# Performance work log

Hardware: AMD Instinct MI355X
Metric: run time of the kernel (lower is better)

## Reference

```python
import jax, jax.numpy as jnp
import numpy as np

B, K, T = 4096, 512, 30
TEMP = 1.0                 # args.score_temp
MAX_GUESSES = 6            # _MAX_GUESSES_NUM
MISS_THRESH = 2.0          # _MISSING_THRESHOLD


def setup_inputs() -> dict:
    key = jax.random.key(0)
    k1, k2, k3, k4 = jax.random.split(key, 4)
    return {
        "output": jax.random.normal(k1, (B * K, 1), dtype=jnp.float32),
        "pred_candidates": jax.random.normal(k2, (B, K, T, 2), dtype=jnp.float32),
        "pred_gt": jax.random.normal(k3, (B, T, 2), dtype=jnp.float32),
        "scales": jax.random.uniform(k4, (B,), dtype=jnp.float32, minval=0.5, maxval=2.0),
    }


def reference(output, pred_candidates, pred_gt, scales):
    out = output.reshape(B, K)                                   # per-sample candidate scores
    # scaled displacement norms: [B, K, T]
    diff = pred_candidates - pred_gt[:, None, :, :]
    disp = scales[:, None, None] * jnp.linalg.norm(diff, axis=-1)
    fde = disp[..., -1]                                          # [B, K] final displacement
    # ScoreEvaluator (FDE metric): higher score = closer endpoint
    scores = -fde
    # classification loss: CE between softmax(target/temp) and log_softmax(output), sum-reduced
    tgt = jax.nn.softmax(scores / TEMP, axis=1)
    logp = jax.nn.log_softmax(out, axis=1)
    cls_loss = -(tgt * logp).sum(axis=1)                         # [B]
    # miss loss: minFDE among top-6 scored candidates, hinged at threshold
    _, top_idx = jax.lax.top_k(out, MAX_GUESSES)                 # [B, 6]
    top_fde = jnp.take_along_axis(fde, top_idx, axis=1)          # [B, 6]
    miss_loss = jnp.maximum(top_fde.min(axis=1) - MISS_THRESH, 0.0)
    return (cls_loss + miss_loss).mean()
```

## Files before the change

kernel.cpp:

```cpp
#include <hip/hip_runtime.h>
#include <cmath>

constexpr int B  = 4096;
constexpr int K  = 512;
constexpr int T  = 30;
constexpr int NT = 256;
constexpr int PT = K / NT;
constexpr int NW = NT / 64;
constexpr int MAX_GUESSES  = 6;
constexpr float MISS_THRESH = 2.0f;

__global__ __launch_bounds__(NT) void score_classify_kernel(
    const float* __restrict__ outp,
    const float* __restrict__ cand,
    const float* __restrict__ gt,
    const float* __restrict__ scales,
    float* __restrict__ part)
{
    const int b    = blockIdx.x;
    const int tid  = threadIdx.x;
    const int wave = tid >> 6;
    const int lane = tid & 63;

    __shared__ float s_fde[K];
    __shared__ float s_red[3 * NW];
    __shared__ int   s_redi[NW];
    __shared__ float s_bcast[2];
    __shared__ int   s_bi;

    const float2 g  = *(const float2*)(gt + ((size_t)b * T + (T - 1)) * 2);
    const float  sc = scales[b];

    float o[PT], f[PT];
#pragma unroll
    for (int j = 0; j < PT; ++j) {
        const int k = tid + j * NT;
        const float2 c = *(const float2*)(cand + (((size_t)(b * K + k)) * T + (T - 1)) * 2);
        const float dx = c.x - g.x;
        const float dy = c.y - g.y;
        f[j] = sc * sqrtf(dx * dx + dy * dy);
        s_fde[k] = f[j];
        o[j] = outp[(size_t)b * K + k];
    }

    float m_o = fmaxf(o[0], o[1]);
    float m_s = fmaxf(-f[0], -f[1]);
    for (int off = 32; off >= 1; off >>= 1) {
        m_o = fmaxf(m_o, __shfl_down(m_o, off));
        m_s = fmaxf(m_s, __shfl_down(m_s, off));
    }
    if (lane == 0) { s_red[wave] = m_o; s_red[NW + wave] = m_s; }
    __syncthreads();
    if (tid == 0) {
        float a = s_red[0], c2 = s_red[NW];
        for (int w = 1; w < NW; ++w) {
            a  = fmaxf(a,  s_red[w]);
            c2 = fmaxf(c2, s_red[NW + w]);
        }
        s_bcast[0] = a; s_bcast[1] = c2;
    }
    __syncthreads();
    m_o = s_bcast[0];
    m_s = s_bcast[1];

    float zo = 0.f, zs = 0.f, ss = 0.f;
#pragma unroll
    for (int j = 0; j < PT; ++j) {
        zo += expf(o[j] - m_o);
        const float e = expf(-f[j] - m_s);
        zs += e;
        ss += e * o[j];
    }
    for (int off = 32; off >= 1; off >>= 1) {
        zo += __shfl_down(zo, off);
        zs += __shfl_down(zs, off);
        ss += __shfl_down(ss, off);
    }
    __syncthreads();
    if (lane == 0) { s_red[wave] = zo; s_red[NW + wave] = zs; s_red[2 * NW + wave] = ss; }
    __syncthreads();
    float cls = 0.f;
    if (tid == 0) {
        float tzo = 0.f, tzs = 0.f, tss = 0.f;
        for (int w = 0; w < NW; ++w) {
            tzo += s_red[w];
            tzs += s_red[NW + w];
            tss += s_red[2 * NW + w];
        }
        cls = m_o + logf(tzo) - tss / tzs;
    }

    bool used[PT];
#pragma unroll
    for (int j = 0; j < PT; ++j) used[j] = false;
    float minfde = 1e30f;

    for (int gidx = 0; gidx < MAX_GUESSES; ++gidx) {
        float bv = -1e30f;
        int   bi = 0x7fffffff;
#pragma unroll
        for (int j = 0; j < PT; ++j) {
            const int k = tid + j * NT;
            if (!used[j] && (o[j] > bv || (o[j] == bv && k < bi))) { bv = o[j]; bi = k; }
        }
        for (int off = 32; off >= 1; off >>= 1) {
            const float v2 = __shfl_down(bv, off);
            const int   i2 = __shfl_down(bi, off);
            if (v2 > bv || (v2 == bv && i2 < bi)) { bv = v2; bi = i2; }
        }
        __syncthreads();
        if (lane == 0) { s_red[wave] = bv; s_redi[wave] = bi; }
        __syncthreads();
        if (tid == 0) {
            float v = s_red[0]; int i = s_redi[0];
            for (int w = 1; w < NW; ++w) {
                if (s_red[w] > v || (s_red[w] == v && s_redi[w] < i)) { v = s_red[w]; i = s_redi[w]; }
            }
            s_bi = i;
        }
        __syncthreads();
        const int widx = s_bi;
        if ((widx & (NT - 1)) == tid) used[widx >> 8] = true;
        minfde = fminf(minfde, s_fde[widx]);
    }

    if (tid == 0) {
        const float miss = fmaxf(minfde - MISS_THRESH, 0.0f);
        part[b] = cls + miss;
    }
}

__global__ __launch_bounds__(NT) void reduce_mean_kernel(
    const float* __restrict__ part,
    float* __restrict__ result)
{
    const int tid  = threadIdx.x;
    const int wave = tid >> 6;
    const int lane = tid & 63;
    __shared__ float s_red[NW];

    float acc = 0.f;
#pragma unroll
    for (int i = tid; i < B; i += NT) acc += part[i];
    for (int off = 32; off >= 1; off >>= 1) acc += __shfl_down(acc, off);
    if (lane == 0) s_red[wave] = acc;
    __syncthreads();
    if (tid == 0) {
        float t = 0.f;
        for (int w = 0; w < NW; ++w) t += s_red[w];
        result[0] = t * (1.0f / (float)B);
    }
}

extern "C" void kernel_launch(void* const* d_in, const int* in_sizes, int n_in,
                              void* d_out, int out_size, void* d_ws, size_t ws_size,
                              hipStream_t stream) {
    const float* outp   = (const float*)d_in[0];
    const float* cand   = (const float*)d_in[1];
    const float* gt     = (const float*)d_in[2];
    const float* scales = (const float*)d_in[3];
    float* result = (float*)d_out;
    float* part   = (float*)d_ws;

    score_classify_kernel<<<B, NT, 0, stream>>>(outp, cand, gt, scales, part);
    reduce_mean_kernel<<<1, NT, 0, stream>>>(part, result);
}
```

Before: 617.2 us.

## Use one wavefront per sample with shuffle-only reductions and register top-k

The score kernel moves from a 256-thread block to a single 64-lane wavefront per sample, with 8 candidates per lane. All reductions (max, sums, the six top-k argmax rounds) become xor-shuffle butterflies, which removes the shared-memory staging and every __syncthreads. The winning candidate's FDE is fetched from registers with a lane shuffle instead of from a shared array. In exchange each lane does more serial work, and there are only 64 threads per block to hide the latency of the scattered 8-byte endpoint loads.

```diff
diff --git a/kernel.cpp b/kernel.cpp
--- a/kernel.cpp
+++ b/kernel.cpp
@@ -4,9 +4,8 @@
 constexpr int B  = 4096;
 constexpr int K  = 512;
 constexpr int T  = 30;
-constexpr int NT = 256;
+constexpr int NT = 64;
 constexpr int PT = K / NT;
-constexpr int NW = NT / 64;
 constexpr int MAX_GUESSES  = 6;
 constexpr float MISS_THRESH = 2.0f;
 
@@ -18,50 +17,39 @@
     float* __restrict__ part)
 {
     const int b    = blockIdx.x;
-    const int tid  = threadIdx.x;
-    const int wave = tid >> 6;
-    const int lane = tid & 63;
-
-    __shared__ float s_fde[K];
-    __shared__ float s_red[3 * NW];
-    __shared__ int   s_redi[NW];
-    __shared__ float s_bcast[2];
-    __shared__ int   s_bi;
+    const int lane = threadIdx.x;
 
     const float2 g  = *(const float2*)(gt + ((size_t)b * T + (T - 1)) * 2);
     const float  sc = scales[b];
 
-    float o[PT], f[PT];
+    float2 c[PT];
+    float  o[PT];
 #pragma unroll
     for (int j = 0; j < PT; ++j) {
-        const int k = tid + j * NT;
-        const float2 c = *(const float2*)(cand + (((size_t)(b * K + k)) * T + (T - 1)) * 2);
-        const float dx = c.x - g.x;
-        const float dy = c.y - g.y;
-        f[j] = sc * sqrtf(dx * dx + dy * dy);
-        s_fde[k] = f[j];
+        const int k = lane + j * NT;
+        c[j] = *(const float2*)(cand + (((size_t)(b * K + k)) * T + (T - 1)) * 2);
         o[j] = outp[(size_t)b * K + k];
     }
 
-    float m_o = fmaxf(o[0], o[1]);
-    float m_s = fmaxf(-f[0], -f[1]);
+    float f[PT];
+#pragma unroll
+    for (int j = 0; j < PT; ++j) {
+        const float dx = c[j].x - g.x;
+        const float dy = c[j].y - g.y;
+        f[j] = sc * sqrtf(dx * dx + dy * dy);
+    }
+
+    float m_o = o[0], m_s = -f[0];
+#pragma unroll
+    for (int j = 1; j < PT; ++j) {
+        m_o = fmaxf(m_o, o[j]);
+        m_s = fmaxf(m_s, -f[j]);
+    }
+#pragma unroll
     for (int off = 32; off >= 1; off >>= 1) {
-        m_o = fmaxf(m_o, __shfl_down(m_o, off));
-        m_s = fmaxf(m_s, __shfl_down(m_s, off));
+        m_o = fmaxf(m_o, __shfl_xor(m_o, off));
+        m_s = fmaxf(m_s, __shfl_xor(m_s, off));
     }
-    if (lane == 0) { s_red[wave] = m_o; s_red[NW + wave] = m_s; }
-    __syncthreads();
-    if (tid == 0) {
-        float a = s_red[0], c2 = s_red[NW];
-        for (int w = 1; w < NW; ++w) {
-            a  = fmaxf(a,  s_red[w]);
-            c2 = fmaxf(c2, s_red[NW + w]);
-        }
-        s_bcast[0] = a; s_bcast[1] = c2;
-    }
-    __syncthreads();
-    m_o = s_bcast[0];
-    m_s = s_bcast[1];
 
     float zo = 0.f, zs = 0.f, ss = 0.f;
 #pragma unroll
@@ -71,28 +59,15 @@
         zs += e;
         ss += e * o[j];
     }
+#pragma unroll
     for (int off = 32; off >= 1; off >>= 1) {
-        zo += __shfl_down(zo, off);
-        zs += __shfl_down(zs, off);
-        ss += __shfl_down(ss, off);
+        zo += __shfl_xor(zo, off);
+        zs += __shfl_xor(zs, off);
+        ss += __shfl_xor(ss, off);
     }
-    __syncthreads();
-    if (lane == 0) { s_red[wave] = zo; s_red[NW + wave] = zs; s_red[2 * NW + wave] = ss; }
-    __syncthreads();
-    float cls = 0.f;
-    if (tid == 0) {
-        float tzo = 0.f, tzs = 0.f, tss = 0.f;
-        for (int w = 0; w < NW; ++w) {
-            tzo += s_red[w];
-            tzs += s_red[NW + w];
-            tss += s_red[2 * NW + w];
-        }
-        cls = m_o + logf(tzo) - tss / tzs;
-    }
+    const float cls = m_o + logf(zo) - ss / zs;
 
-    bool used[PT];
-#pragma unroll
-    for (int j = 0; j < PT; ++j) used[j] = false;
+    unsigned used = 0;
     float minfde = 1e30f;
 
     for (int gidx = 0; gidx < MAX_GUESSES; ++gidx) {
@@ -100,54 +75,51 @@
         int   bi = 0x7fffffff;
 #pragma unroll
         for (int j = 0; j < PT; ++j) {
-            const int k = tid + j * NT;
-            if (!used[j] && (o[j] > bv || (o[j] == bv && k < bi))) { bv = o[j]; bi = k; }
+            const int k = lane + j * NT;
+            const bool ok = !(used & (1u << j));
+            if (ok && (o[j] > bv || (o[j] == bv && k < bi))) { bv = o[j]; bi = k; }
         }
+#pragma unroll
         for (int off = 32; off >= 1; off >>= 1) {
-            const float v2 = __shfl_down(bv, off);
-            const int   i2 = __shfl_down(bi, off);
+            const float v2 = __shfl_xor(bv, off);
+            const int   i2 = __shfl_xor(bi, off);
             if (v2 > bv || (v2 == bv && i2 < bi)) { bv = v2; bi = i2; }
         }
-        __syncthreads();
-        if (lane == 0) { s_red[wave] = bv; s_redi[wave] = bi; }
-        __syncthreads();
-        if (tid == 0) {
-            float v = s_red[0]; int i = s_redi[0];
-            for (int w = 1; w < NW; ++w) {
-                if (s_red[w] > v || (s_red[w] == v && s_redi[w] < i)) { v = s_red[w]; i = s_redi[w]; }
-            }
-            s_bi = i;
-        }
-        __syncthreads();
-        const int widx = s_bi;
-        if ((widx & (NT - 1)) == tid) used[widx >> 8] = true;
-        minfde = fminf(minfde, s_fde[widx]);
+        const int owner = bi & (NT - 1);
+        const int jw    = bi >> 6;
+        if (lane == owner) used |= (1u << jw);
+        float fv = f[0];
+#pragma unroll
+        for (int j = 1; j < PT; ++j) if (j == jw) fv = f[j];
+        const float wfde = __shfl(fv, owner);
+        minfde = fminf(minfde, wfde);
     }
 
-    if (tid == 0) {
+    if (lane == 0) {
         const float miss = fmaxf(minfde - MISS_THRESH, 0.0f);
         part[b] = cls + miss;
     }
 }
 
-__global__ __launch_bounds__(NT) void reduce_mean_kernel(
+__global__ __launch_bounds__(256) void reduce_mean_kernel(
     const float* __restrict__ part,
     float* __restrict__ result)
 {
     const int tid  = threadIdx.x;
     const int wave = tid >> 6;
     const int lane = tid & 63;
-    __shared__ float s_red[NW];
+    __shared__ float s_red[4];
 
     float acc = 0.f;
 #pragma unroll
-    for (int i = tid; i < B; i += NT) acc += part[i];
+    for (int i = tid; i < B; i += 256) acc += part[i];
+#pragma unroll
     for (int off = 32; off >= 1; off >>= 1) acc += __shfl_down(acc, off);
     if (lane == 0) s_red[wave] = acc;
     __syncthreads();
     if (tid == 0) {
         float t = 0.f;
-        for (int w = 0; w < NW; ++w) t += s_red[w];
+        for (int w = 0; w < 4; ++w) t += s_red[w];
         result[0] = t * (1.0f / (float)B);
     }
 }
@@ -163,5 +135,5 @@
     float* part   = (float*)d_ws;
 
     score_classify_kernel<<<B, NT, 0, stream>>>(outp, cand, gt, scales, part);
-    reduce_mean_kernel<<<1, NT, 0, stream>>>(part, result);
+    reduce_mean_kernel<<<1, 256, 0, stream>>>(part, result);
 }
```

Result: no change. 612.1 us (-0.8%).
